# Performance work log

Measured on AMD Instinct MI355X. Metric: run time of the kernel, lower is better.

## Reference

```python
import jax, jax.numpy as jnp
import numpy as np

B, T, E = 64, 64, 512
D_MODEL = 2 * E          # 1024, mamba d_model (concat of spatial+temporal)
D_INNER = 2 * D_MODEL    # 2048
D_STATE = 16
DT_RANK = D_MODEL // 16  # 64
K_CONV = 4


def setup_inputs() -> dict:
    key = jax.random.key(0)
    ks = jax.random.split(key, 12)
    def n(k, shape, scale=0.02):
        return jax.random.normal(k, shape, jnp.float32) * scale
    return {
        "spatial_features": jax.random.normal(ks[0], (B, T, E), jnp.float32),
        "temporal_features": jax.random.normal(ks[1], (B, T, E), jnp.float32),
        "W_in": n(ks[2], (D_MODEL, 2 * D_INNER)),
        "conv_w": n(ks[3], (D_INNER, K_CONV)),
        "conv_b": jnp.zeros((D_INNER,), jnp.float32),
        "W_x": n(ks[4], (D_INNER, DT_RANK + 2 * D_STATE)),
        "W_dt": n(ks[5], (DT_RANK, D_INNER)),
        "b_dt": jnp.zeros((D_INNER,), jnp.float32),
        "A_log": n(ks[6], (D_INNER, D_STATE)),   # A = -exp(A_log) ~ -1
        "D_skip": jnp.ones((D_INNER,), jnp.float32),
        "W_out": n(ks[7], (D_INNER, D_MODEL)),
        "W1": n(ks[8], (D_MODEL, 512)),
        "b1": jnp.zeros((512,), jnp.float32),
        "W2": n(ks[9], (512, 256)),
        "b2": jnp.zeros((256,), jnp.float32),
        "W3": n(ks[10], (256, 6)),
        "b3": jnp.zeros((6,), jnp.float32),
    }


def _mamba(x, W_in, conv_w, conv_b, W_x, W_dt, b_dt, A_log, D_skip, W_out):
    # x: (B, T, d_model) -> (B, T, d_model). Standard Mamba selective-scan block.
    Bsz = x.shape[0]
    xz = jnp.einsum('btd,de->bte', x, W_in)            # (B,T,2*d_inner)
    xi, z = jnp.split(xz, 2, axis=-1)
    # causal depthwise conv1d over T
    xt = jnp.pad(jnp.swapaxes(xi, 1, 2), ((0, 0), (0, 0), (K_CONV - 1, 0)))
    conv = jax.lax.conv_general_dilated(
        xt, conv_w[:, None, :], (1,), 'VALID', feature_group_count=D_INNER)
    xc = jax.nn.silu(jnp.swapaxes(conv, 1, 2) + conv_b)  # (B,T,d_inner)
    proj = jnp.einsum('btd,de->bte', xc, W_x)            # (B,T,dt_rank+2n)
    dt_raw, Bs, Cs = jnp.split(proj, [DT_RANK, DT_RANK + D_STATE], axis=-1)
    dt = jax.nn.softplus(jnp.einsum('btr,rd->btd', dt_raw, W_dt) + b_dt)
    A = -jnp.exp(A_log)                                  # (d_inner, n)

    def step(h, inputs):
        dt_t, B_t, C_t, x_t = inputs                     # (B,d),(B,n),(B,n),(B,d)
        dA = jnp.exp(dt_t[..., None] * A)                # (B,d,n)
        h = dA * h + (dt_t * x_t)[..., None] * B_t[:, None, :]
        y = jnp.einsum('bdn,bn->bd', h, C_t)
        return h, y

    xs = (jnp.swapaxes(dt, 0, 1), jnp.swapaxes(Bs, 0, 1),
          jnp.swapaxes(Cs, 0, 1), jnp.swapaxes(xc, 0, 1))
    h0 = jnp.zeros((Bsz, D_INNER, D_STATE), xc.dtype)
    _, ys = jax.lax.scan(step, h0, xs)
    y = jnp.swapaxes(ys, 0, 1) + xc * D_skip
    y = y * jax.nn.silu(z)
    return jnp.einsum('btd,de->bte', y, W_out)


def reference(spatial_features, temporal_features, W_in, conv_w, conv_b, W_x,
              W_dt, b_dt, A_log, D_skip, W_out, W1, b1, W2, b2, W3, b3):
    # concat -> final Mamba -> per-frame MLP head (vectorized over B,T)
    x = jnp.concatenate([spatial_features, temporal_features], axis=-1)  # (B,T,2E)
    f = _mamba(x, W_in, conv_w, conv_b, W_x, W_dt, b_dt, A_log, D_skip, W_out)
    h1 = jax.nn.relu(f @ W1 + b1)
    h2 = jax.nn.relu(h1 @ W2 + b2)
    return h2 @ W3 + b3  # (B,T,6)
```

## Files before the change

kernel.cpp:

```cpp
#include <hip/hip_runtime.h>
#include <hip/hip_bf16.h>
#include <math.h>

#define B_   64
#define T_   64
#define E_   512
#define DM   1024
#define DI   2048
#define DS   16
#define DTR  64
#define M_   4096

typedef __hip_bfloat16 bf16;
typedef __attribute__((ext_vector_type(8))) short bf16x8;
typedef __attribute__((ext_vector_type(4))) float f32x4;

__device__ __forceinline__ float b2f(short s) {
    return __uint_as_float(((unsigned)(unsigned short)s) << 16);
}

template<int ACT, int OUTBF, int SPLITK, int BM, int BN>
__global__ __launch_bounds__(256) void gemm_mfma(
    const bf16* __restrict__ A, int lda,
    const bf16* __restrict__ Bt, int ldb,
    void* __restrict__ Cv, int ldc,
    const float* __restrict__ bias,
    int Ndim, int Kdim)
{
    __shared__ __align__(16) bf16 As[BM * 32];
    __shared__ __align__(16) bf16 Bs[BN * 32];
    const int tid  = threadIdx.x;
    const int wave = tid >> 6;
    const int lane = tid & 63;
    const int bm = blockIdx.y * BM;
    const int bn = blockIdx.x * BN;
    const int lrow = lane >> 2;
    const int lkc  = (lane & 3) * 8;
    constexpr int RPW = (BM + BN) / 4;
    constexpr int NI  = RPW / 16;
    constexpr int WMT = BM / 32;
    constexpr int WNT = BN / 32;
    const int wm = (wave >> 1) * (BM / 2);
    const int wn = (wave & 1) * (BN / 2);
    const int fm = lane & 15;
    const int fq = lane >> 4;

    int kstart = 0, kend = Kdim;
    if (SPLITK > 1) {
        int chunk = Kdim / SPLITK;
        kstart = blockIdx.z * chunk;
        kend = kstart + chunk;
    }

    f32x4 acc[WMT][WNT];
    #pragma unroll
    for (int i = 0; i < WMT; ++i)
        #pragma unroll
        for (int j = 0; j < WNT; ++j)
            acc[i][j] = (f32x4){0.f, 0.f, 0.f, 0.f};

    for (int k0 = kstart; k0 < kend; k0 += 32) {
        #pragma unroll
        for (int i = 0; i < NI; ++i) {
            int rowbase = wave * RPW + i * 16;
            int row = rowbase + lrow;
            if (rowbase < BM) {
                const bf16* ga = A + (size_t)(bm + row) * lda + k0 + lkc;
                __builtin_amdgcn_global_load_lds(
                    (const __attribute__((address_space(1))) void*)ga,
                    (__attribute__((address_space(3))) void*)&As[rowbase * 32],
                    16, 0, 0);
            } else {
                int brow = bn + row - BM;
                if (brow >= Ndim) brow = Ndim - 1;
                const bf16* gb = Bt + (size_t)brow * ldb + k0 + lkc;
                __builtin_amdgcn_global_load_lds(
                    (const __attribute__((address_space(1))) void*)gb,
                    (__attribute__((address_space(3))) void*)&Bs[(rowbase - BM) * 32],
                    16, 0, 0);
            }
        }
        __syncthreads();
        bf16x8 a[WMT], b[WNT];
        #pragma unroll
        for (int i = 0; i < WMT; ++i)
            a[i] = *(const bf16x8*)&As[(wm + i * 16 + fm) * 32 + fq * 8];
        #pragma unroll
        for (int j = 0; j < WNT; ++j)
            b[j] = *(const bf16x8*)&Bs[(wn + j * 16 + fm) * 32 + fq * 8];
        #pragma unroll
        for (int i = 0; i < WMT; ++i)
            #pragma unroll
            for (int j = 0; j < WNT; ++j)
                acc[i][j] = __builtin_amdgcn_mfma_f32_16x16x32_bf16(
                    a[i], b[j], acc[i][j], 0, 0, 0);
        __syncthreads();
    }

    size_t zoff = (SPLITK > 1) ? (size_t)blockIdx.z * M_ * ldc : 0;
    #pragma unroll
    for (int i = 0; i < WMT; ++i) {
        int rowb = bm + wm + i * 16 + fq * 4;
        #pragma unroll
        for (int j = 0; j < WNT; ++j) {
            int col = bn + wn + j * 16 + fm;
            if (col < Ndim) {
                float bv = bias ? bias[col] : 0.f;
                #pragma unroll
                for (int r = 0; r < 4; ++r) {
                    float v = acc[i][j][r] + bv;
                    if (ACT == 1) v = fmaxf(v, 0.f);
                    if (ACT == 2) v = (v > 20.f) ? v : __logf(1.f + __expf(v));
                    size_t off = (size_t)(rowb + r) * ldc + col;
                    if (SPLITK > 1) ((float*)Cv)[zoff + off] = v;
                    else if (OUTBF) ((bf16*)Cv)[off] = __float2bfloat16(v);
                    else            ((float*)Cv)[off] = v;
                }
            }
        }
    }
}

__global__ __launch_bounds__(256) void gemm_g1_conv(
    const bf16* __restrict__ A,
    const bf16* __restrict__ Bt,
    bf16* __restrict__ xcb,
    bf16* __restrict__ zb,
    const float* __restrict__ conv_w,
    const float* __restrict__ conv_b)
{
    constexpr int XS = 136;
    __shared__ __align__(16) bf16 smem[128 * XS];
    const int tid  = threadIdx.x;
    const int wave = tid >> 6;
    const int lane = tid & 63;
    const int bm = blockIdx.y * 128;
    const int bn = blockIdx.x * 128;
    const int lrow = lane >> 2;
    const int lkc  = (lane & 3) * 8;
    const int wm = (wave >> 1) * 64;
    const int wn = (wave & 1) * 64;
    const int fm = lane & 15;
    const int fq = lane >> 4;

    f32x4 acc[4][4];
    #pragma unroll
    for (int i = 0; i < 4; ++i)
        #pragma unroll
        for (int j = 0; j < 4; ++j)
            acc[i][j] = (f32x4){0.f, 0.f, 0.f, 0.f};

    for (int k0 = 0; k0 < 1024; k0 += 32) {
        #pragma unroll
        for (int i = 0; i < 4; ++i) {
            int rowbase = wave * 64 + i * 16;
            int row = rowbase + lrow;
            if (rowbase < 128) {
                const bf16* ga = A + (size_t)(bm + row) * 1024 + k0 + lkc;
                __builtin_amdgcn_global_load_lds(
                    (const __attribute__((address_space(1))) void*)ga,
                    (__attribute__((address_space(3))) void*)&smem[rowbase * 32],
                    16, 0, 0);
            } else {
                const bf16* gb = Bt + (size_t)(bn + row - 128) * 1024 + k0 + lkc;
                __builtin_amdgcn_global_load_lds(
                    (const __attribute__((address_space(1))) void*)gb,
                    (__attribute__((address_space(3))) void*)&smem[4096 + (rowbase - 128) * 32],
                    16, 0, 0);
            }
        }
        __syncthreads();
        bf16x8 a[4], b[4];
        #pragma unroll
        for (int i = 0; i < 4; ++i)
            a[i] = *(const bf16x8*)&smem[(wm + i * 16 + fm) * 32 + fq * 8];
        #pragma unroll
        for (int j = 0; j < 4; ++j)
            b[j] = *(const bf16x8*)&smem[4096 + (wn + j * 16 + fm) * 32 + fq * 8];
        #pragma unroll
        for (int i = 0; i < 4; ++i)
            #pragma unroll
            for (int j = 0; j < 4; ++j)
                acc[i][j] = __builtin_amdgcn_mfma_f32_16x16x32_bf16(
                    a[i], b[j], acc[i][j], 0, 0, 0);
        __syncthreads();
    }

    if (bn < 2048) {
        #pragma unroll
        for (int i = 0; i < 4; ++i) {
            int rowb = wm + i * 16 + fq * 4;
            #pragma unroll
            for (int j = 0; j < 4; ++j) {
                int col = wn + j * 16 + fm;
                #pragma unroll
                for (int r = 0; r < 4; ++r)
                    smem[(rowb + r) * XS + col] = __float2bfloat16(acc[i][j][r]);
            }
        }
        __syncthreads();
        {
            int col = tid & 127;
            int seq = tid >> 7;
            int gcol = bn + col;
            float4 cw = *(const float4*)&conv_w[gcol * 4];
            float cb = conv_b[gcol];
            float w0 = 0.f, w1 = 0.f, w2 = 0.f;
            int base = seq * 64;
            for (int t = 0; t < 64; ++t) {
                int idx = (base + t) * XS + col;
                float cur = __bfloat162float(smem[idx]);
                float cacc = cb;
                cacc = fmaf(w0, cw.x, cacc); cacc = fmaf(w1, cw.y, cacc);
                cacc = fmaf(w2, cw.z, cacc); cacc = fmaf(cur, cw.w, cacc);
                smem[idx] = __float2bfloat16(__fdividef(cacc, 1.f + __expf(-cacc)));
                w0 = w1; w1 = w2; w2 = cur;
            }
        }
        __syncthreads();
        #pragma unroll
        for (int it = 0; it < 8; ++it) {
            int g = it * 256 + tid;
            int row = g >> 4;
            int cg = (g & 15) * 8;
            bf16x8 v = *(const bf16x8*)&smem[row * XS + cg];
            *(bf16x8*)&xcb[(size_t)(bm + row) * 2048 + bn + cg] = v;
        }
    } else {
        #pragma unroll
        for (int i = 0; i < 4; ++i) {
            int rowb = bm + wm + i * 16 + fq * 4;
            #pragma unroll
            for (int j = 0; j < 4; ++j) {
                int col = bn - 2048 + wn + j * 16 + fm;
                #pragma unroll
                for (int r = 0; r < 4; ++r)
                    zb[(size_t)(rowb + r) * 2048 + col] =
                        __float2bfloat16(acc[i][j][r]);
            }
        }
    }
}

template<int P, int RELU, int NCOL>
__global__ __launch_bounds__(256) void redp_kernel(
    const float* __restrict__ parts, int stride,
    const float* __restrict__ bias, bf16* __restrict__ out)
{
    int i4 = blockIdx.x * 256 + threadIdx.x;
    int i = i4 * 4;
    float4 s = *(const float4*)(parts + i);
    #pragma unroll
    for (int p = 1; p < P; ++p) {
        float4 v = *(const float4*)(parts + (size_t)p * stride + i);
        s.x += v.x; s.y += v.y; s.z += v.z; s.w += v.w;
    }
    if (NCOL > 0) {
        int c = i & (NCOL - 1);
        s.x += bias[c]; s.y += bias[c + 1]; s.z += bias[c + 2]; s.w += bias[c + 3];
    }
    if (RELU) {
        s.x = fmaxf(s.x, 0.f); s.y = fmaxf(s.y, 0.f);
        s.z = fmaxf(s.z, 0.f); s.w = fmaxf(s.w, 0.f);
    }
    bf16 o[4] = {__float2bfloat16(s.x), __float2bfloat16(s.y),
                 __float2bfloat16(s.z), __float2bfloat16(s.w)};
    *(short4*)&out[i] = *(short4*)o;
}

template<int P>
__global__ __launch_bounds__(256) void reduce_proj_kernel(
    const float* __restrict__ parts, float* __restrict__ proj,
    bf16* __restrict__ projb)
{
    int i = blockIdx.x * 256 + threadIdx.x;
    float s = parts[i];
    #pragma unroll
    for (int p = 1; p < P; ++p) s += parts[(size_t)p * 393216 + i];
    proj[i] = s;
    projb[i] = __float2bfloat16(s);
}

__global__ __launch_bounds__(256) void prep_kernel(
    const float* __restrict__ sp, const float* __restrict__ tp,
    bf16* __restrict__ xb,
    const float* __restrict__ W_in,  bf16* __restrict__ WinT,
    const float* __restrict__ W_x,   bf16* __restrict__ WxT,
    const float* __restrict__ W_dt,  bf16* __restrict__ WdT,
    const float* __restrict__ W_out, bf16* __restrict__ WoT,
    const float* __restrict__ W1,    bf16* __restrict__ W1T,
    const float* __restrict__ W2,    bf16* __restrict__ W2T)
{
    __shared__ float tile[32][33];
    const int b = blockIdx.x;
    const int tid = threadIdx.x;
    if (b < 4096) {
        int idx = b * 256 + tid;
        int row = idx >> 8;
        int c4 = (idx & 255) * 4;
        const float* src = (c4 < 512) ? (sp + (size_t)row * 512 + c4)
                                      : (tp + (size_t)row * 512 + (c4 - 512));
        float4 v = *(const float4*)src;
        bf16* dst = xb + (size_t)row * 1024 + c4;
        dst[0] = __float2bfloat16(v.x); dst[1] = __float2bfloat16(v.y);
        dst[2] = __float2bfloat16(v.z); dst[3] = __float2bfloat16(v.w);
        return;
    }
    const float* W; bf16* Wt; int K, N, tb;
    if      (b < 8192)  { W = W_in;  Wt = WinT; K = 1024; N = 4096; tb = b - 4096; }
    else if (b < 8384)  { W = W_x;   Wt = WxT;  K = 2048; N = 96;   tb = b - 8192; }
    else if (b < 8512)  { W = W_dt;  Wt = WdT;  K = 64;   N = 2048; tb = b - 8384; }
    else if (b < 10560) { W = W_out; Wt = WoT;  K = 2048; N = 1024; tb = b - 8512; }
    else if (b < 11072) { W = W1;    Wt = W1T;  K = 1024; N = 512;  tb = b - 10560; }
    else                { W = W2;    Wt = W2T;  K = 512;  N = 256;  tb = b - 11072; }
    int nb = N / 32;
    int bn = (tb % nb) * 32, bk = (tb / nb) * 32;
    int tx = tid & 31, ty = tid >> 5;
    #pragma unroll
    for (int i = 0; i < 32; i += 8)
        tile[ty + i][tx] = W[(size_t)(bk + ty + i) * N + bn + tx];
    __syncthreads();
    #pragma unroll
    for (int i = 0; i < 32; i += 8)
        Wt[(size_t)(bn + ty + i) * K + bk + tx] = __float2bfloat16(tile[tx][ty + i]);
}

__global__ __launch_bounds__(256) void scan_kernel(
    const float* __restrict__ proj,
    const bf16*  __restrict__ dtb,
    bf16* __restrict__ xcy,
    const bf16*  __restrict__ zb,
    const float* __restrict__ A_log,
    const float* __restrict__ D_skip)
{
    __shared__ float BC[64][32];
    const int tid = threadIdx.x;
    const int b = blockIdx.y;
    for (int i = tid; i < 64 * 32; i += 256) {
        int t = i >> 5, c = i & 31;
        BC[t][c] = proj[(size_t)(b * 64 + t) * 96 + 64 + c];
    }
    __syncthreads();

    const int d = blockIdx.x * 256 + tid;
    float av[16];
    const float4* alp = (const float4*)(A_log + d * 16);
    *(float4*)&av[0]  = alp[0];
    *(float4*)&av[4]  = alp[1];
    *(float4*)&av[8]  = alp[2];
    *(float4*)&av[12] = alp[3];
    float A[16];
    #pragma unroll
    for (int n = 0; n < 16; ++n) A[n] = -__expf(av[n]);
    const float Dv = D_skip[d];
    float h[16];
    #pragma unroll
    for (int n = 0; n < 16; ++n) h[n] = 0.f;

    #pragma unroll 2
    for (int t = 0; t < T_; ++t) {
        int row = b * T_ + t;
        size_t off = (size_t)row * DI + d;
        float xv = __bfloat162float(xcy[off]);
        float dt = __bfloat162float(dtb[off]);
        float dtx = dt * xv;
        float y = 0.f;
        #pragma unroll
        for (int n = 0; n < 16; ++n) {
            float dA = __expf(dt * A[n]);
            h[n] = fmaf(dA, h[n], dtx * BC[t][n]);
            y = fmaf(h[n], BC[t][16 + n], y);
        }
        float sk = fmaf(xv, Dv, y);
        float z = __bfloat162float(zb[off]);
        float g = __fdividef(z, 1.f + __expf(-z));
        xcy[off] = __float2bfloat16(sk * g);
    }
}

template<int P>
__global__ __launch_bounds__(256) void head_kernel(
    const float* __restrict__ p6, int stride,
    const float* __restrict__ b2,
    const float* __restrict__ W3, const float* __restrict__ b3,
    float* __restrict__ out)
{
    int row = blockIdx.x * 4 + (threadIdx.x >> 6);
    int lane = threadIdx.x & 63;
    float acc[6] = {0.f, 0.f, 0.f, 0.f, 0.f, 0.f};
    #pragma unroll
    for (int kk = 0; kk < 4; ++kk) {
        int c = lane + kk * 64;
        size_t off = (size_t)row * 256 + c;
        float s = p6[off];
        #pragma unroll
        for (int p = 1; p < P; ++p) s += p6[(size_t)p * stride + off];
        s = fmaxf(s + b2[c], 0.f);
        #pragma unroll
        for (int n = 0; n < 6; ++n) acc[n] = fmaf(s, W3[c * 6 + n], acc[n]);
    }
    #pragma unroll
    for (int n = 0; n < 6; ++n) {
        float v = acc[n];
        #pragma unroll
        for (int off = 32; off > 0; off >>= 1) v += __shfl_down(v, off);
        if (lane == 0) out[(size_t)row * 6 + n] = v + b3[n];
    }
}

extern "C" void kernel_launch(void* const* d_in, const int* in_sizes, int n_in,
                              void* d_out, int out_size, void* d_ws, size_t ws_size,
                              hipStream_t stream)
{
    const float* spatial  = (const float*)d_in[0];
    const float* temporal = (const float*)d_in[1];
    const float* W_in     = (const float*)d_in[2];
    const float* conv_w   = (const float*)d_in[3];
    const float* conv_b   = (const float*)d_in[4];
    const float* W_x      = (const float*)d_in[5];
    const float* W_dt     = (const float*)d_in[6];
    const float* b_dt     = (const float*)d_in[7];
    const float* A_log    = (const float*)d_in[8];
    const float* D_skip   = (const float*)d_in[9];
    const float* W_out    = (const float*)d_in[10];
    const float* W1       = (const float*)d_in[11];
    const float* b1       = (const float*)d_in[12];
    const float* W2       = (const float*)d_in[13];
    const float* b2       = (const float*)d_in[14];
    const float* W3       = (const float*)d_in[15];
    const float* b3       = (const float*)d_in[16];
    float* out = (float*)d_out;

    char* w = (char*)d_ws;
    bf16*  xcb  = (bf16*)(w);
    bf16*  f    = (bf16*)(w);
    bf16*  zb   = (bf16*)(w + 16777216);
    bf16*  dtb  = (bf16*)(w + 33554432);
    float* p4   = (float*)(w + 33554432);
    float* p5   = (float*)(w + 33554432);
    float* p6   = (float*)(w + 33554432);
    bf16*  xb   = (bf16*)(w + 67108864);
    bf16*  WinT = (bf16*)(w + 75497472);
    bf16*  WoT  = (bf16*)(w + 83886080);
    bf16*  W1T  = (bf16*)(w + 88080384);
    bf16*  W2T  = (bf16*)(w + 89128960);
    bf16*  WxT  = (bf16*)(w + 89391104);
    bf16*  WdT  = (bf16*)(w + 89784320);
    float* projp= (float*)(w + 90046464);
    float* proj = (float*)(w + 102629376);
    bf16*  projb= (bf16*)(w + 104202240);
    bf16*  h1   = (bf16*)(w + 104988672);

    dim3 blk(256);

    prep_kernel<<<dim3(11200), blk, 0, stream>>>(
        spatial, temporal, xb, W_in, WinT, W_x, WxT, W_dt, WdT,
        W_out, WoT, W1, W1T, W2, W2T);

    gemm_g1_conv<<<dim3(32, 32), blk, 0, stream>>>(
        xb, WinT, xcb, zb, conv_w, conv_b);

    gemm_mfma<0, 0, 8, 128, 128><<<dim3(1, 32, 8), blk, 0, stream>>>(
        xcb, 2048, WxT, 2048, projp, 96, nullptr, 96, 2048);

    reduce_proj_kernel<8><<<dim3(1536), blk, 0, stream>>>(projp, proj, projb);

    gemm_mfma<2, 1, 1, 128, 64><<<dim3(32, 32), blk, 0, stream>>>(
        projb, 96, WdT, 64, dtb, 2048, b_dt, 2048, 64);

    scan_kernel<<<dim3(8, 64), blk, 0, stream>>>(
        proj, dtb, xcb, zb, A_log, D_skip);

    gemm_mfma<0, 0, 2, 128, 128><<<dim3(8, 32, 2), blk, 0, stream>>>(
        xcb, 2048, WoT, 2048, p4, 1024, nullptr, 1024, 2048);

    redp_kernel<2, 0, 0><<<dim3(4096), blk, 0, stream>>>(
        p4, 4194304, nullptr, f);

    gemm_mfma<0, 0, 4, 128, 128><<<dim3(4, 32, 4), blk, 0, stream>>>(
        f, 1024, W1T, 1024, p5, 512, nullptr, 512, 1024);

    redp_kernel<4, 1, 512><<<dim3(2048), blk, 0, stream>>>(
        p5, 2097152, b1, h1);

    gemm_mfma<0, 0, 4, 128, 128><<<dim3(2, 32, 4), blk, 0, stream>>>(
        h1, 512, W2T, 512, p6, 256, nullptr, 256, 512);

    head_kernel<4><<<dim3(1024), blk, 0, stream>>>(
        p6, 1048576, b2, W3, b3, out);
}
```

Before: 321.0 us.

## Fold W_out into W1 to skip out-projection GEMM and intermediate

Since the Mamba output f feeds straight into f@W1 with no nonlinearity between them, the code precomputes a combined weight (W_out·W1, transposed, 2048x512) with a small GEMM on the weights. The scan output is then multiplied directly by it. This removes the 4096x2048x1024 out-projection GEMM, its split-K reduction kernel and the f buffer. It adds a 512x2048x1024 weight GEMM per call, a separate transpose kernel for W_in, and an extra bf16 rounding of the combined weight.

Result: faster. 304.1 us (-5.3%).

```diff
diff --git a/kernel.cpp b/kernel.cpp
--- a/kernel.cpp
+++ b/kernel.cpp
@@ -284,10 +284,9 @@
 __global__ __launch_bounds__(256) void prep_kernel(
     const float* __restrict__ sp, const float* __restrict__ tp,
     bf16* __restrict__ xb,
-    const float* __restrict__ W_in,  bf16* __restrict__ WinT,
+    const float* __restrict__ W_out, bf16* __restrict__ Wob,
     const float* __restrict__ W_x,   bf16* __restrict__ WxT,
     const float* __restrict__ W_dt,  bf16* __restrict__ WdT,
-    const float* __restrict__ W_out, bf16* __restrict__ WoT,
     const float* __restrict__ W1,    bf16* __restrict__ W1T,
     const float* __restrict__ W2,    bf16* __restrict__ W2T)
 {
@@ -306,13 +305,19 @@
         dst[2] = __float2bfloat16(v.z); dst[3] = __float2bfloat16(v.w);
         return;
     }
+    if (b < 6144) {
+        int idx = (b - 4096) * 1024 + tid * 4;
+        float4 v = *(const float4*)(W_out + idx);
+        bf16 o[4] = {__float2bfloat16(v.x), __float2bfloat16(v.y),
+                     __float2bfloat16(v.z), __float2bfloat16(v.w)};
+        *(short4*)&Wob[idx] = *(short4*)o;
+        return;
+    }
     const float* W; bf16* Wt; int K, N, tb;
-    if      (b < 8192)  { W = W_in;  Wt = WinT; K = 1024; N = 4096; tb = b - 4096; }
-    else if (b < 8384)  { W = W_x;   Wt = WxT;  K = 2048; N = 96;   tb = b - 8192; }
-    else if (b < 8512)  { W = W_dt;  Wt = WdT;  K = 64;   N = 2048; tb = b - 8384; }
-    else if (b < 10560) { W = W_out; Wt = WoT;  K = 2048; N = 1024; tb = b - 8512; }
-    else if (b < 11072) { W = W1;    Wt = W1T;  K = 1024; N = 512;  tb = b - 10560; }
-    else                { W = W2;    Wt = W2T;  K = 512;  N = 256;  tb = b - 11072; }
+    if      (b < 6336) { W = W_x;  Wt = WxT; K = 2048; N = 96;   tb = b - 6144; }
+    else if (b < 6464) { W = W_dt; Wt = WdT; K = 64;   N = 2048; tb = b - 6336; }
+    else if (b < 6976) { W = W1;   Wt = W1T; K = 1024; N = 512;  tb = b - 6464; }
+    else               { W = W2;   Wt = W2T; K = 512;  N = 256;  tb = b - 6976; }
     int nb = N / 32;
     int bn = (tb % nb) * 32, bk = (tb / nb) * 32;
     int tx = tid & 31, ty = tid >> 5;
@@ -433,15 +438,13 @@
 
     char* w = (char*)d_ws;
     bf16*  xcb  = (bf16*)(w);
-    bf16*  f    = (bf16*)(w);
     bf16*  zb   = (bf16*)(w + 16777216);
     bf16*  dtb  = (bf16*)(w + 33554432);
-    float* p4   = (float*)(w + 33554432);
     float* p5   = (float*)(w + 33554432);
     float* p6   = (float*)(w + 33554432);
     bf16*  xb   = (bf16*)(w + 67108864);
     bf16*  WinT = (bf16*)(w + 75497472);
-    bf16*  WoT  = (bf16*)(w + 83886080);
+    bf16*  WcT  = (bf16*)(w + 83886080);
     bf16*  W1T  = (bf16*)(w + 88080384);
     bf16*  W2T  = (bf16*)(w + 89128960);
     bf16*  WxT  = (bf16*)(w + 89391104);
@@ -450,12 +453,21 @@
     float* proj = (float*)(w + 102629376);
     bf16*  projb= (bf16*)(w + 104202240);
     bf16*  h1   = (bf16*)(w + 104988672);
+    bf16*  Wob  = (bf16*)(w + 109182976);
 
     dim3 blk(256);
 
-    prep_kernel<<<dim3(11200), blk, 0, stream>>>(
-        spatial, temporal, xb, W_in, WinT, W_x, WxT, W_dt, WdT,
-        W_out, WoT, W1, W1T, W2, W2T);
+    prep_kernel<<<dim3(7104), blk, 0, stream>>>(
+        spatial, temporal, xb, W_out, Wob, W_x, WxT, W_dt, WdT,
+        W1, W1T, W2, W2T);
+
+    {
+        extern __global__ void tconv_win(const float*, bf16*);
+        tconv_win<<<dim3(4096), blk, 0, stream>>>(W_in, WinT);
+    }
+
+    gemm_mfma<0, 1, 1, 128, 64><<<dim3(32, 4), blk, 0, stream>>>(
+        W1T, 1024, Wob, 1024, WcT, 2048, nullptr, 2048, 1024);
 
     gemm_g1_conv<<<dim3(32, 32), blk, 0, stream>>>(
         xb, WinT, xcb, zb, conv_w, conv_b);
@@ -471,14 +483,8 @@
     scan_kernel<<<dim3(8, 64), blk, 0, stream>>>(
         proj, dtb, xcb, zb, A_log, D_skip);
 
-    gemm_mfma<0, 0, 2, 128, 128><<<dim3(8, 32, 2), blk, 0, stream>>>(
-        xcb, 2048, WoT, 2048, p4, 1024, nullptr, 1024, 2048);
-
-    redp_kernel<2, 0, 0><<<dim3(4096), blk, 0, stream>>>(
-        p4, 4194304, nullptr, f);
-
     gemm_mfma<0, 0, 4, 128, 128><<<dim3(4, 32, 4), blk, 0, stream>>>(
-        f, 1024, W1T, 1024, p5, 512, nullptr, 512, 1024);
+        xcb, 2048, WcT, 2048, p5, 512, nullptr, 512, 2048);
 
     redp_kernel<4, 1, 512><<<dim3(2048), blk, 0, stream>>>(
         p5, 2097152, b1, h1);
@@ -489,3 +495,20 @@
     head_kernel<4><<<dim3(1024), blk, 0, stream>>>(
         p6, 1048576, b2, W3, b3, out);
 }
+
+__global__ __launch_bounds__(256) void tconv_win(
+    const float* __restrict__ W, bf16* __restrict__ Wt)
+{
+    __shared__ float tile[32][33];
+    int tb = blockIdx.x;
+    int bn = (tb & 127) * 32;
+    int bk = (tb >> 7) * 32;
+    int tx = threadIdx.x & 31, ty = threadIdx.x >> 5;
+    #pragma unroll
+    for (int i = 0; i < 32; i += 8)
+        tile[ty + i][tx] = W[(size_t)(bk + ty + i) * 4096 + bn + tx];
+    __syncthreads();
+    #pragma unroll
+    for (int i = 0; i < 32; i += 8)
+        Wt[(size_t)(bn + ty + i) * 1024 + bk + tx] = __float2bfloat16(tile[tx][ty + i]);
+}
```
